# Kernel optimization log

Measured on AMD Instinct MI355X. Metric: run time of the kernel, lower is better.

Reference implementation:

```python
import jax, jax.numpy as jnp
import numpy as np

NP_, NC_, E_, F_, D_, O_ = 50000, 100000, 600000, 69, 128, 2


def _embed(x, shift, scale, w1, b1, w2, b2):
    # PreNormLayer (shift+scale) -> Linear -> ReLU -> Linear -> ReLU
    x = (x + shift) * scale
    return jax.nn.relu(jax.nn.relu(x @ w1 + b1) @ w2 + b2)


def _biconv(left, src, dst, right, wl, bl, wr, sf, wf, bf, sp, wo1, bo1, wo2, bo2):
    # message: final( left_mod(right[dst]) + right_mod(left[src]) ), mean-scatter to dst
    pre = (right[dst] @ wl + bl) + left[src] @ wr            # [E, D]
    msg = jax.nn.relu(pre * sf) @ wf + bf                    # [E, D]
    n = right.shape[0]
    sums = jax.ops.segment_sum(msg, dst, num_segments=n)     # [N_right, D]
    cnt = jax.ops.segment_sum(jnp.ones((dst.shape[0], 1), msg.dtype), dst, num_segments=n)
    agg = sums / jnp.maximum(cnt, 1.0)
    h = jnp.concatenate([agg * sp, right], axis=-1)          # [N_right, 2D]
    return jax.nn.relu(h @ wo1 + bo1) @ wo2 + bo2


def setup_inputs():
    key = jax.random.key(0)
    ks = jax.random.split(key, 40)
    it = iter(range(4, 40))
    def nw(shape):
        return (jax.random.normal(ks[next(it)], shape, dtype=jnp.float32) * 0.05)
    inp = {}
    inp['pivot_features'] = jax.random.normal(ks[0], (NP_, F_), dtype=jnp.float32)
    inp['children_features'] = jax.random.normal(ks[1], (NC_, F_), dtype=jnp.float32)
    src = jax.random.randint(ks[2], (E_,), 0, NP_, dtype=jnp.int32)
    dst = jax.random.randint(ks[3], (E_,), 0, NC_, dtype=jnp.int32)
    inp['edge_indices'] = jnp.stack([src, dst], axis=0)
    # pivot / children embedding MLPs (PreNorm buffers at init values)
    for p in ('pe', 'ce'):
        inp[p + '_shift'] = jnp.zeros((F_,), jnp.float32)
        inp[p + '_scale'] = jnp.ones((F_,), jnp.float32)
        inp[p + '_w1'] = nw((F_, D_)); inp[p + '_b1'] = jnp.zeros((D_,), jnp.float32)
        inp[p + '_w2'] = nw((D_, D_)); inp[p + '_b2'] = jnp.zeros((D_,), jnp.float32)
    # two bipartite conv layers
    for p in ('vc', 'cv'):
        inp[p + '_wl'] = nw((D_, D_)); inp[p + '_bl'] = jnp.zeros((D_,), jnp.float32)
        inp[p + '_wr'] = nw((D_, D_))
        inp[p + '_sf'] = jnp.ones((1,), jnp.float32)   # PreNormLayer(1, shift=False) scale
        inp[p + '_wf'] = nw((D_, D_)); inp[p + '_bf'] = jnp.zeros((D_,), jnp.float32)
        inp[p + '_sp'] = jnp.ones((1,), jnp.float32)   # post_conv PreNormLayer scale
        inp[p + '_wo1'] = nw((2 * D_, D_)); inp[p + '_bo1'] = jnp.zeros((D_,), jnp.float32)
        inp[p + '_wo2'] = nw((D_, D_)); inp[p + '_bo2'] = jnp.zeros((D_,), jnp.float32)
    inp['out_w1'] = nw((D_, D_)); inp['out_b1'] = jnp.zeros((D_,), jnp.float32)
    inp['out_w2'] = nw((D_, O_)); inp['out_b2'] = jnp.zeros((O_,), jnp.float32)
    return inp


def reference(pivot_features, children_features, edge_indices,
              pe_shift, pe_scale, pe_w1, pe_b1, pe_w2, pe_b2,
              ce_shift, ce_scale, ce_w1, ce_b1, ce_w2, ce_b2,
              vc_wl, vc_bl, vc_wr, vc_sf, vc_wf, vc_bf, vc_sp, vc_wo1, vc_bo1, vc_wo2, vc_bo2,
              cv_wl, cv_bl, cv_wr, cv_sf, cv_wf, cv_bf, cv_sp, cv_wo1, cv_bo1, cv_wo2, cv_bo2,
              out_w1, out_b1, out_w2, out_b2):
    pv = _embed(pivot_features, pe_shift, pe_scale, pe_w1, pe_b1, pe_w2, pe_b2)
    ch = _embed(children_features, ce_shift, ce_scale, ce_w1, ce_b1, ce_w2, ce_b2)
    src, dst = edge_indices[0], edge_indices[1]
    # conv_v_to_c: left=pivot, right=children, aggregate to children
    ch = _biconv(pv, src, dst, ch, vc_wl, vc_bl, vc_wr, vc_sf, vc_wf, vc_bf, vc_sp,
                 vc_wo1, vc_bo1, vc_wo2, vc_bo2)
    # conv_c_to_v with reversed edges: left=children, right=pivot, aggregate to pivot
    pv = _biconv(ch, dst, src, pv, cv_wl, cv_bl, cv_wr, cv_sf, cv_wf, cv_bf, cv_sp,
                 cv_wo1, cv_bo1, cv_wo2, cv_bo2)
    return jax.nn.sigmoid(jax.nn.relu(pv @ out_w1 + out_b1) @ out_w2 + out_b2)
```

## Files before the change

kernel.cpp:

```cpp
#include <hip/hip_runtime.h>
#include <math.h>


typedef unsigned short u16;
typedef __attribute__((ext_vector_type(8))) short s8v;
typedef __attribute__((ext_vector_type(4))) float f4v;

__device__ __forceinline__ float bf2f(u16 u) {
    unsigned x = ((unsigned)u) << 16;
    return __builtin_bit_cast(float, x);
}
__device__ __forceinline__ u16 f2bf(float f) {
    unsigned x = __builtin_bit_cast(unsigned, f);
    unsigned r = x + 0x7fffu + ((x >> 16) & 1u);
    return (u16)(r >> 16);
}
__device__ __forceinline__ void unpack8(uint4 u, float* f) {
    f[0] = bf2f((u16)(u.x & 0xffff)); f[1] = bf2f((u16)(u.x >> 16));
    f[2] = bf2f((u16)(u.y & 0xffff)); f[3] = bf2f((u16)(u.y >> 16));
    f[4] = bf2f((u16)(u.z & 0xffff)); f[5] = bf2f((u16)(u.z >> 16));
    f[6] = bf2f((u16)(u.w & 0xffff)); f[7] = bf2f((u16)(u.w >> 16));
}

struct SmEnt { const float* A; const float* B; const float* s; };
struct SmPack { SmEnt e[4]; };

__global__ __launch_bounds__(256) void smallmm(SmPack p, float* __restrict__ out)
{
    int t = blockIdx.x * 256 + threadIdx.x;
    int m = t >> 14;
    int o = t & 16383;
    int i = o >> 7, j = o & 127;
    SmEnt en = p.e[m];
    float acc = 0.f;
#pragma unroll 4
    for (int k = 0; k < 128; ++k) acc += en.A[i * 128 + k] * en.B[k * 128 + j];
    if (en.s) acc *= *en.s;
    out[(size_t)m * 16384 + o] = acc;
}

__global__ void vecpre(
    const float* vc_bf, const float* vc_wo1, const float* vc_sp,
    const float* cv_bf, const float* cv_wo1, const float* cv_sp,
    const float* vc_bo2, const float* cv_wr,
    const float* cv_bo2, const float* out_w1, const float* out_b1,
    float* __restrict__ vout)
{
    int j = threadIdx.x;
    if (j >= 128) return;
    float a0 = 0.f, a1 = 0.f, a2 = 0.f, a3 = 0.f;
    for (int k = 0; k < 128; ++k) {
        a0 += vc_bf[k] * vc_wo1[k * 128 + j];
        a1 += cv_bf[k] * cv_wo1[k * 128 + j];
        a2 += vc_bo2[k] * cv_wr[k * 128 + j];
        a3 += cv_bo2[k] * out_w1[k * 128 + j];
    }
    vout[j] = a0 * (*vc_sp);
    vout[128 + j] = a1 * (*cv_sp);
    vout[256 + j] = a2;
    vout[384 + j] = a3 + out_b1[j];
}

struct WEnt { const float* src; int Ksrc; int Kdst; };
struct WPack { WEnt e[14]; };

__global__ __launch_bounds__(256) void wconvert(WPack p, u16* __restrict__ wt)
{
    int t = blockIdx.x * 256 + threadIdx.x;
    int m = t >> 15;
    int i = t & 32767;
    WEnt en = p.e[m];
    if (i >= (en.Kdst << 7)) return;
    int k = i >> 7, col = i & 127;
    float v = (k < en.Ksrc) ? en.src[k * 128 + col] : 0.f;
    wt[(size_t)m * 32768 + (size_t)col * en.Kdst + k] = f2bf(v);
}

__global__ __launch_bounds__(256) void featconv(
    const float* __restrict__ x, const float* __restrict__ shift,
    const float* __restrict__ scale, u16* __restrict__ y,
    long total, int F)
{
    for (long i = (long)blockIdx.x * 256 + threadIdx.x; i < total;
         i += (long)gridDim.x * 256) {
        int c = (int)(i % 96);
        long r = i / 96;
        float v = 0.f;
        if (c < F) {
            v = x[r * F + c];
            v = (v + shift[c]) * scale[c];
        }
        y[i] = f2bf(v);
    }
}

template <int KS1, bool HASA2, bool RELU, bool GATE>
__global__ __launch_bounds__(256) void gemm_rb(
    const u16* __restrict__ A1, const u16* __restrict__ A2,
    const u16* __restrict__ WT1,
    const u16* __restrict__ WT2,
    const float* __restrict__ bias0,
    const float* __restrict__ bias1,
    const float* __restrict__ gate,
    u16* __restrict__ out, int M)
{
    constexpr int K1 = KS1 * 32;
    constexpr bool PF = !HASA2;
    constexpr int AS = KS1 + (HASA2 ? 4 : 0);
    const int lane = threadIdx.x & 63;
    const int c = lane & 15;
    const int kg = lane >> 4;
    const int wid = blockIdx.x * 4 + (threadIdx.x >> 6);
    const int ws = gridDim.x * 4;
    const int items = M >> 4;

    const u16* wbase = WT1 + (size_t)c * K1 + kg * 8;
    s8v bp[KS1][8];
#pragma unroll
    for (int ks = 0; ks < KS1; ++ks)
#pragma unroll
        for (int nt = 0; nt < 8; ++nt)
            bp[ks][nt] = *(const s8v*)(wbase + ((size_t)nt * 16) * K1 + ks * 32);

    const u16* wbase2 = HASA2 ? (WT2 + (size_t)c * 128 + kg * 8) : nullptr;

    float bc0[8], bc1[8];
#pragma unroll
    for (int nt = 0; nt < 8; ++nt) {
        bc0[nt] = bias0 ? bias0[nt * 16 + c] : 0.f;
        bc1[nt] = (GATE && bias1) ? bias1[nt * 16 + c] : 0.f;
    }

    auto lda = [&](s8v* a, int item) {
        const u16* ap = A1 + (size_t)((item << 4) + c) * K1 + kg * 8;
#pragma unroll
        for (int ks = 0; ks < KS1; ++ks) a[ks] = *(const s8v*)(ap + ks * 32);
        if (HASA2) {
            const u16* ap2 = A2 + (size_t)((item << 4) + c) * 128 + kg * 8;
#pragma unroll
            for (int ks = 0; ks < 4; ++ks) a[KS1 + ks] = *(const s8v*)(ap2 + ks * 32);
        }
    };

    s8v a[AS], an[AS], a2[AS];
    int item = wid;
    if (item < items) lda(a, item);
    if (PF && item + ws < items) lda(an, item + ws);
    while (item < items) {
        const int i2 = item + 2 * ws;
        if (PF && i2 < items) lda(a2, i2);

        f4v acc[8];
#pragma unroll
        for (int nt = 0; nt < 8; ++nt) acc[nt] = (f4v){0.f, 0.f, 0.f, 0.f};
#pragma unroll
        for (int ks = 0; ks < KS1; ++ks)
#pragma unroll
            for (int nt = 0; nt < 8; ++nt)
                acc[nt] = __builtin_amdgcn_mfma_f32_16x16x32_bf16(a[ks], bp[ks][nt], acc[nt], 0, 0, 0);
        if (HASA2) {
#pragma unroll
            for (int ks = 0; ks < 4; ++ks)
#pragma unroll
                for (int nt = 0; nt < 8; ++nt) {
                    s8v b = *(const s8v*)(wbase2 + ((size_t)nt * 16) * 128 + ks * 32);
                    acc[nt] = __builtin_amdgcn_mfma_f32_16x16x32_bf16(a[KS1 + ks], b, acc[nt], 0, 0, 0);
                }
        }

        const int r0 = item << 4;
        float g4[4];
#pragma unroll
        for (int j = 0; j < 4; ++j)
            g4[j] = GATE ? (gate[r0 + kg * 4 + j] > 0.f ? 1.f : 0.f) : 0.f;
#pragma unroll
        for (int nt = 0; nt < 8; ++nt)
#pragma unroll
            for (int j = 0; j < 4; ++j) {
                float v = acc[nt][j] + bc0[nt] + g4[j] * bc1[nt];
                if (RELU) v = fmaxf(v, 0.f);
                out[(size_t)(r0 + kg * 4 + j) * 128 + nt * 16 + c] = f2bf(v);
            }

        if (PF) {
#pragma unroll
            for (int ks = 0; ks < AS; ++ks) { a[ks] = an[ks]; an[ks] = a2[ks]; }
        } else if (item + ws < items) {
            lda(a, item + ws);
        }
        item += ws;
    }
}

__global__ __launch_bounds__(256) void head_fused(
    const u16* __restrict__ A1, const u16* __restrict__ WT,
    const float* __restrict__ b1, const float* __restrict__ w2,
    const float* __restrict__ b2, float* __restrict__ outp, int M)
{
    constexpr int KT = 128;
    const int lane = threadIdx.x & 63;
    const int c = lane & 15;
    const int kg = lane >> 4;
    const int wid = blockIdx.x * 4 + (threadIdx.x >> 6);
    const int ws = gridDim.x * 4;
    const int items = M >> 4;

    const u16* wbase = WT + (size_t)c * KT + kg * 8;
    s8v bp[4][8];
#pragma unroll
    for (int ks = 0; ks < 4; ++ks)
#pragma unroll
        for (int nt = 0; nt < 8; ++nt)
            bp[ks][nt] = *(const s8v*)(wbase + ((size_t)nt * 16) * KT + ks * 32);

    float bc[8], w2c0[8], w2c1[8];
#pragma unroll
    for (int nt = 0; nt < 8; ++nt) {
        int col = nt * 16 + c;
        bc[nt] = b1[col];
        w2c0[nt] = w2[col * 2 + 0];
        w2c1[nt] = w2[col * 2 + 1];
    }
    const float s0 = b2[0], s1 = b2[1];

    for (int item = wid; item < items; item += ws) {
        const int r0 = item << 4;
        const u16* ap = A1 + (size_t)(r0 + c) * 128 + kg * 8;
        s8v a[4];
#pragma unroll
        for (int ks = 0; ks < 4; ++ks) a[ks] = *(const s8v*)(ap + ks * 32);

        f4v acc[8];
#pragma unroll
        for (int nt = 0; nt < 8; ++nt) acc[nt] = (f4v){0.f, 0.f, 0.f, 0.f};
#pragma unroll
        for (int ks = 0; ks < 4; ++ks)
#pragma unroll
            for (int nt = 0; nt < 8; ++nt)
                acc[nt] = __builtin_amdgcn_mfma_f32_16x16x32_bf16(a[ks], bp[ks][nt], acc[nt], 0, 0, 0);

        float pp0[4] = {0.f, 0.f, 0.f, 0.f}, pp1[4] = {0.f, 0.f, 0.f, 0.f};
#pragma unroll
        for (int nt = 0; nt < 8; ++nt)
#pragma unroll
            for (int j = 0; j < 4; ++j) {
                float v = fmaxf(acc[nt][j] + bc[nt], 0.f);
                pp0[j] += v * w2c0[nt];
                pp1[j] += v * w2c1[nt];
            }
#pragma unroll
        for (int m = 1; m < 16; m <<= 1)
#pragma unroll
            for (int j = 0; j < 4; ++j) {
                pp0[j] += __shfl_xor(pp0[j], m);
                pp1[j] += __shfl_xor(pp1[j], m);
            }
        if (c == 0) {
#pragma unroll
            for (int j = 0; j < 4; ++j) {
                int row = r0 + kg * 4 + j;
                outp[(size_t)row * 2 + 0] = 1.f / (1.f + expf(-(pp0[j] + s0)));
                outp[(size_t)row * 2 + 1] = 1.f / (1.f + expf(-(pp1[j] + s1)));
            }
        }
    }
}


__global__ __launch_bounds__(256) void binA(
    const int* __restrict__ src, const int* __restrict__ dst,
    int E, int CH, int NB, int nbk_c, int NBK,
    int* __restrict__ G, int* __restrict__ Tb)
{
    __shared__ int h[1024];
    const int blk = blockIdx.x, tid = threadIdx.x;
    for (int i = tid; i < NBK; i += 256) h[i] = 0;
    __syncthreads();
    const int e0 = blk * CH, e1 = min(E, e0 + CH);
    for (int e = e0 + tid; e < e1; e += 256) {
        atomicAdd(&h[dst[e] >> 9], 1);
        atomicAdd(&h[nbk_c + (src[e] >> 9)], 1);
    }
    __syncthreads();
    for (int b = tid; b < NBK; b += 256) {
        const int v = h[b];
        G[b * NB + blk] = v;
        if (v) atomicAdd(&Tb[b], v);
    }
}

__global__ __launch_bounds__(512) void binS(
    const int* __restrict__ Tb, int NBK, int* __restrict__ BB)
{
    __shared__ int wsum[8];
    const int tid = threadIdx.x;
    const int T = (tid < NBK) ? Tb[tid] : 0;
    const int lane = tid & 63, wv = tid >> 6;
    int incl = T;
#pragma unroll
    for (int d = 1; d < 64; d <<= 1) {
        int up = __shfl_up(incl, d);
        if (lane >= d) incl += up;
    }
    if (lane == 63) wsum[wv] = incl;
    __syncthreads();
    if (tid == 0) {
        int run = 0;
        for (int w = 0; w < 8; ++w) { int t = wsum[w]; wsum[w] = run; run += t; }
    }
    __syncthreads();
    const int base = wsum[wv] + incl - T;
    if (tid < NBK) {
        BB[tid] = base;
        if (tid == NBK - 1) BB[NBK] = base + T;
    }
}

__global__ __launch_bounds__(64) void binP(
    const int* __restrict__ G, const int* __restrict__ BB,
    int NB, int* __restrict__ PBB)
{
    const int b = blockIdx.x, l = threadIdx.x;
    const int* g = G + (size_t)b * NB;
    const int v0 = (l < NB) ? g[l] : 0;
    const int v1 = (l + 64 < NB) ? g[l + 64] : 0;
    int i0 = v0, i1 = v1;
#pragma unroll
    for (int d = 1; d < 64; d <<= 1) {
        int u0 = __shfl_up(i0, d);
        int u1 = __shfl_up(i1, d);
        if (l >= d) { i0 += u0; i1 += u1; }
    }
    const int t0 = __shfl(i0, 63);
    const int base = BB[b];
    int* p = PBB + (size_t)b * NB;
    if (l < NB) p[l] = base + i0 - v0;
    if (l + 64 < NB) p[l + 64] = base + t0 + i1 - v1;
}

__global__ __launch_bounds__(256) void binB(
    const int* __restrict__ src, const int* __restrict__ dst,
    int E, int CH, int NB, int nbk_c, int NBK,
    const int* __restrict__ PBB, unsigned* __restrict__ REC)
{
    __shared__ int fill[1024];
    const int blk = blockIdx.x, tid = threadIdx.x;
    for (int i = tid; i < NBK; i += 256) fill[i] = 0;
    __syncthreads();
    const int e0 = blk * CH, e1 = min(E, e0 + CH);
    for (int e = e0 + tid; e < e1; e += 256) {
        const int s = src[e], d = dst[e];
        const int bc = d >> 9;
        const int pc = PBB[bc * NB + blk] + atomicAdd(&fill[bc], 1);
        REC[pc] = (unsigned)s | ((unsigned)(d & 511) << 17);
        const int bp = nbk_c + (s >> 9);
        const int pp = PBB[bp * NB + blk] + atomicAdd(&fill[bp], 1);
        REC[pp] = (unsigned)d | ((unsigned)(s & 511) << 17);
    }
}

__global__ __launch_bounds__(256) void binC(
    const unsigned* __restrict__ REC, const int* __restrict__ BB,
    int bucket_base, int Nn,
    int* __restrict__ off_out, int* __restrict__ cnt_out, int* __restrict__ AJ)
{
    __shared__ int nh[512], lo[512], fl[512], ws2[4];
    const int b = blockIdx.x, tid = threadIdx.x;
    const int gb = bucket_base + b;
    const int r0 = BB[gb], r1 = BB[gb + 1];
    const int node0 = b << 9;
    const int kmax = min(512, Nn - node0);
    nh[tid] = 0; nh[tid + 256] = 0;
    fl[tid] = 0; fl[tid + 256] = 0;
    __syncthreads();
    for (int i = r0 + tid; i < r1; i += 256)
        atomicAdd(&nh[REC[i] >> 17], 1);
    __syncthreads();
    const int v0 = nh[2 * tid], v1 = nh[2 * tid + 1];
    const int s = v0 + v1;
    const int lane = tid & 63, wv = tid >> 6;
    int incl = s;
#pragma unroll
    for (int d = 1; d < 64; d <<= 1) {
        int up = __shfl_up(incl, d);
        if (lane >= d) incl += up;
    }
    if (lane == 63) ws2[wv] = incl;
    __syncthreads();
    if (tid == 0) {
        int run = 0;
        for (int w = 0; w < 4; ++w) { int t = ws2[w]; ws2[w] = run; run += t; }
    }
    __syncthreads();
    const int base = ws2[wv] + incl - s;
    lo[2 * tid] = base;
    lo[2 * tid + 1] = base + v0;
    __syncthreads();
    for (int k = tid; k < kmax; k += 256) {
        off_out[node0 + k] = r0 + lo[k];
        cnt_out[node0 + k] = nh[k];
    }
    for (int i = r0 + tid; i < r1; i += 256) {
        const unsigned rec = REC[i];
        const int k = rec >> 17;
        const int pos = r0 + lo[k] + atomicAdd(&fl[k], 1);
        AJ[pos] = (int)(rec & 0x1FFFFu);
    }
}

__global__ __launch_bounds__(256) void node_gather2(
    const int* __restrict__ off, const int* __restrict__ cnt,
    const int* __restrict__ adj,
    const u16* __restrict__ RW, const u16* __restrict__ LW,
    u16* __restrict__ Sdiv, float* __restrict__ cntf,
    const float* __restrict__ sf_p, int N)
{
    int t = blockIdx.x * 256 + threadIdx.x;
    int n = t >> 5;
    if (n >= N) return;
    int l32 = t & 31;
    int c = l32 & 15;
    int half = l32 >> 4;
    const float sf = *sf_p;
    const int start = off[n], len = cnt[n];

    float rw[8];
    unpack8(*(const uint4*)(RW + (size_t)n * 128 + c * 8), rw);
    float acc[8] = {0.f, 0.f, 0.f, 0.f, 0.f, 0.f, 0.f, 0.f};

    for (int i = half; i < len; i += 2) {
        int l = adj[start + i];
        float lw[8];
        unpack8(*(const uint4*)(LW + (size_t)l * 128 + c * 8), lw);
#pragma unroll
        for (int j = 0; j < 8; ++j)
            acc[j] += fmaxf((rw[j] + lw[j]) * sf, 0.f);
    }
#pragma unroll
    for (int j = 0; j < 8; ++j) acc[j] += __shfl_xor(acc[j], 16);

    if (half == 0) {
        float inv = 1.f / fmaxf((float)len, 1.f);
        uint4 o;
        o.x = (unsigned)f2bf(acc[0] * inv) | ((unsigned)f2bf(acc[1] * inv) << 16);
        o.y = (unsigned)f2bf(acc[2] * inv) | ((unsigned)f2bf(acc[3] * inv) << 16);
        o.z = (unsigned)f2bf(acc[4] * inv) | ((unsigned)f2bf(acc[5] * inv) << 16);
        o.w = (unsigned)f2bf(acc[6] * inv) | ((unsigned)f2bf(acc[7] * inv) << 16);
        *(uint4*)(Sdiv + (size_t)n * 128 + c * 8) = o;
        if (l32 == 0) cntf[n] = (float)len;
    }
}

extern "C" void kernel_launch(void* const* d_in, const int* in_sizes, int n_in,
                              void* d_out, int out_size, void* d_ws, size_t ws_size,
                              hipStream_t stream)
{
    const float* pivot = (const float*)d_in[0];
    const float* child = (const float*)d_in[1];
    const int* edges = (const int*)d_in[2];
    const int F = in_sizes[3];
    const int NP = in_sizes[0] / F;
    const int NC = in_sizes[1] / F;
    const int E = in_sizes[2] / 2;
    const int* src = edges;
    const int* dst = edges + E;

    const float *pe_shift = (const float*)d_in[3], *pe_scale = (const float*)d_in[4],
                *pe_w1 = (const float*)d_in[5], *pe_b1 = (const float*)d_in[6],
                *pe_w2 = (const float*)d_in[7], *pe_b2 = (const float*)d_in[8];
    const float *ce_shift = (const float*)d_in[9], *ce_scale = (const float*)d_in[10],
                *ce_w1 = (const float*)d_in[11], *ce_b1 = (const float*)d_in[12],
                *ce_w2 = (const float*)d_in[13], *ce_b2 = (const float*)d_in[14];
    const float *vc_wl = (const float*)d_in[15], *vc_bl = (const float*)d_in[16],
                *vc_wr = (const float*)d_in[17], *vc_sf = (const float*)d_in[18],
                *vc_wf = (const float*)d_in[19], *vc_bf = (const float*)d_in[20],
                *vc_sp = (const float*)d_in[21], *vc_wo1 = (const float*)d_in[22],
                *vc_bo1 = (const float*)d_in[23], *vc_wo2 = (const float*)d_in[24],
                *vc_bo2 = (const float*)d_in[25];
    const float *cv_wl = (const float*)d_in[26], *cv_bl = (const float*)d_in[27],
                *cv_wr = (const float*)d_in[28], *cv_sf = (const float*)d_in[29],
                *cv_wf = (const float*)d_in[30], *cv_bf = (const float*)d_in[31],
                *cv_sp = (const float*)d_in[32], *cv_wo1 = (const float*)d_in[33],
                *cv_bo1 = (const float*)d_in[34], *cv_wo2 = (const float*)d_in[35],
                *cv_bo2 = (const float*)d_in[36];
    const float *out_w1 = (const float*)d_in[37], *out_b1 = (const float*)d_in[38],
                *out_w2 = (const float*)d_in[39], *out_b2 = (const float*)d_in[40];

    char* base = (char*)d_ws;
    size_t off = 0;
    auto carve = [&](size_t bytes) {
        void* p = base + off;
        off += (bytes + 255) & ~(size_t)255;
        return p;
    };
    float* Wsc = (float*)carve((size_t)4 * 16384 * 4);
    float* Vsc = (float*)carve((size_t)4 * 128 * 4);
    u16* WT = (u16*)carve((size_t)14 * 32768 * 2);
    u16* FP = (u16*)carve((size_t)NP * 96 * 2);
    u16* FC = (u16*)carve((size_t)NC * 96 * 2);
    u16* B0 = (u16*)carve((size_t)NP * 128 * 2);
    u16* B1 = (u16*)carve((size_t)NC * 128 * 2);
    u16* B2 = (u16*)carve((size_t)NC * 128 * 2);
    u16* B3 = (u16*)carve((size_t)NC * 128 * 2);
    u16* B4 = (u16*)carve((size_t)NC * 128 * 2);
    const int NMAX = (NC > NP) ? NC : NP;
    float* cntf = (float*)carve((size_t)NMAX * 4);

    const int NB = 120;
    const int CH = (E + NB - 1) / NB;
    const int nbk_c = (NC + 511) >> 9;
    const int nbk_p = (NP + 511) >> 9;
    const int NBK = nbk_c + nbk_p;
    int* cnt_c = (int*)carve((size_t)NC * 4);
    int* cnt_p = (int*)carve((size_t)NP * 4);
    int* off_c = (int*)carve((size_t)NC * 4);
    int* off_p = (int*)carve((size_t)NP * 4);
    int* G = (int*)carve((size_t)NBK * NB * 4);
    int* PBB = (int*)carve((size_t)NBK * NB * 4);
    int* BB = (int*)carve((size_t)(NBK + 1) * 4);
    int* Tb = (int*)carve((size_t)NBK * 4);
    unsigned* REC = (unsigned*)carve((size_t)2 * E * 4);
    int* AJ = (int*)carve((size_t)2 * E * 4);

    SmPack sp;
    sp.e[0] = {vc_wf, vc_wo1, vc_sp};
    sp.e[1] = {cv_wf, cv_wo1, cv_sp};
    sp.e[2] = {vc_wo2, cv_wr, nullptr};
    sp.e[3] = {cv_wo2, out_w1, nullptr};
    hipLaunchKernelGGL(smallmm, dim3(256), dim3(256), 0, stream, sp, Wsc);
    hipLaunchKernelGGL(vecpre, dim3(1), dim3(128), 0, stream,
                       vc_bf, vc_wo1, vc_sp, cv_bf, cv_wo1, cv_sp,
                       vc_bo2, cv_wr, cv_bo2, out_w1, out_b1, Vsc);
    const float* cvec_vc = Vsc;
    const float* cvec_cv = Vsc + 128;
    const float* cx = Vsc + 256;
    const float* bh = Vsc + 384;

    WPack wp;
    auto setw = [&](int i, const float* s, int ks, int kd) {
        wp.e[i].src = s; wp.e[i].Ksrc = ks; wp.e[i].Kdst = kd;
    };
    setw(0, pe_w1, F, 96);            setw(1, pe_w2, 128, 128);
    setw(2, ce_w1, F, 96);            setw(3, ce_w2, 128, 128);
    setw(4, vc_wl, 128, 128);         setw(5, vc_wr, 128, 128);
    setw(6, Wsc + 0 * 16384, 128, 128);
    setw(7, vc_wo1 + 128 * 128, 128, 128);
    setw(8, Wsc + 2 * 16384, 128, 128);
    setw(9, cv_wl, 128, 128);         setw(10, cv_wr, 128, 128);
    setw(11, Wsc + 1 * 16384, 128, 128);
    setw(12, cv_wo1 + 128 * 128, 128, 128);
    setw(13, Wsc + 3 * 16384, 128, 128);
    hipLaunchKernelGGL(wconvert, dim3(14 * 128), dim3(256), 0, stream, wp, WT);
    auto wt = [&](int i) { return WT + (size_t)i * 32768; };

    hipLaunchKernelGGL(featconv, dim3(2048), dim3(256), 0, stream,
                       pivot, pe_shift, pe_scale, FP, (long)NP * 96, F);
    hipLaunchKernelGGL(featconv, dim3(2048), dim3(256), 0, stream,
                       child, ce_shift, ce_scale, FC, (long)NC * 96, F);

    hipMemsetAsync(Tb, 0, (size_t)NBK * 4, stream);
    hipLaunchKernelGGL(binA, dim3(NB), dim3(256), 0, stream,
                       src, dst, E, CH, NB, nbk_c, NBK, G, Tb);
    hipLaunchKernelGGL(binS, dim3(1), dim3(512), 0, stream, Tb, NBK, BB);
    hipLaunchKernelGGL(binP, dim3(NBK), dim3(64), 0, stream, G, BB, NB, PBB);
    hipLaunchKernelGGL(binB, dim3(NB), dim3(256), 0, stream,
                       src, dst, E, CH, NB, nbk_c, NBK, PBB, REC);
    hipLaunchKernelGGL(binC, dim3(nbk_c), dim3(256), 0, stream,
                       REC, BB, 0, NC, off_c, cnt_c, AJ);
    hipLaunchKernelGGL(binC, dim3(nbk_p), dim3(256), 0, stream,
                       REC, BB, nbk_c, NP, off_p, cnt_p, AJ);

    const dim3 blk(256);
    auto grd = [](int M) {
        int items = M >> 4;
        int b = (items + 3) / 4;
        return dim3((unsigned)(b < 512 ? b : 512));
    };

    gemm_rb<3, false, true, false><<<grd(NP), blk, 0, stream>>>(
        FP, nullptr, wt(0), nullptr, pe_b1, nullptr, nullptr, B1, NP);
    gemm_rb<4, false, true, false><<<grd(NP), blk, 0, stream>>>(
        B1, nullptr, wt(1), nullptr, pe_b2, nullptr, nullptr, B0, NP);
    gemm_rb<3, false, true, false><<<grd(NC), blk, 0, stream>>>(
        FC, nullptr, wt(2), nullptr, ce_b1, nullptr, nullptr, B1, NC);
    gemm_rb<4, false, true, false><<<grd(NC), blk, 0, stream>>>(
        B1, nullptr, wt(3), nullptr, ce_b2, nullptr, nullptr, B2, NC);

    gemm_rb<4, false, false, false><<<grd(NC), blk, 0, stream>>>(
        B2, nullptr, wt(4), nullptr, vc_bl, nullptr, nullptr, B1, NC);
    gemm_rb<4, false, false, false><<<grd(NP), blk, 0, stream>>>(
        B0, nullptr, wt(5), nullptr, nullptr, nullptr, nullptr, B3, NP);
    hipLaunchKernelGGL(node_gather2, dim3(((size_t)NC * 32 + 255) / 256), blk, 0,
                       stream, off_c, cnt_c, AJ, B1, B3, B4, cntf, vc_sf, NC);
    gemm_rb<4, true, true, true><<<grd(NC), blk, 0, stream>>>(
        B4, B2, wt(6), wt(7), vc_bo1, cvec_vc, cntf, B1, NC);
    gemm_rb<4, false, false, false><<<grd(NC), blk, 0, stream>>>(
        B1, nullptr, wt(8), nullptr, cx, nullptr, nullptr, B3, NC);

    gemm_rb<4, false, false, false><<<grd(NP), blk, 0, stream>>>(
        B0, nullptr, wt(9), nullptr, cv_bl, nullptr, nullptr, B2, NP);
    hipLaunchKernelGGL(node_gather2, dim3(((size_t)NP * 32 + 255) / 256), blk, 0,
                       stream, off_p, cnt_p, AJ, B2, B3, B4, cntf, cv_sf, NP);
    gemm_rb<4, true, true, true><<<grd(NP), blk, 0, stream>>>(
        B4, B0, wt(11), wt(12), cv_bo1, cvec_cv, cntf, B1, NP);

    hipLaunchKernelGGL(head_fused, grd(NP), blk, 0, stream,
                       B1, wt(13), bh, out_w2, out_b2, (float*)d_out, NP);
}
```

Before: 362.0 us.

## Batch independent GEMMs into multi-job launches and transpose MFMA for packed stores

Independent per-node GEMMs (pivot and children embeddings, and the three projection GEMMs) are grouped into single launches using blockIdx.y as a job selector. The two feature-conversion kernels and the two binC kernels are merged the same way, which cuts launch count and improves GPU fill for the smaller pivot jobs. The MFMA operands are swapped so each lane holds four consecutive output columns, allowing packed 8-byte bf16 stores and vector bias loads instead of scattered 2-byte stores. Extra buffers are allocated to avoid aliasing between the now-concurrent jobs.

After: 373.7 us. +3.2%, slower.

```diff
diff --git a/kernel.cpp b/kernel.cpp
--- a/kernel.cpp
+++ b/kernel.cpp
@@ -14,6 +14,9 @@
     unsigned x = __builtin_bit_cast(unsigned, f);
     unsigned r = x + 0x7fffu + ((x >> 16) & 1u);
     return (u16)(r >> 16);
+}
+__device__ __forceinline__ unsigned pk2(float a, float b) {
+    return (unsigned)f2bf(a) | ((unsigned)f2bf(b) << 16);
 }
 __device__ __forceinline__ void unpack8(uint4 u, float* f) {
     f[0] = bf2f((u16)(u.x & 0xffff)); f[1] = bf2f((u16)(u.x >> 16));
@@ -76,19 +79,24 @@
     wt[(size_t)m * 32768 + (size_t)col * en.Kdst + k] = f2bf(v);
 }
 
-__global__ __launch_bounds__(256) void featconv(
-    const float* __restrict__ x, const float* __restrict__ shift,
-    const float* __restrict__ scale, u16* __restrict__ y,
-    long total, int F)
+__global__ __launch_bounds__(256) void featconv2(
+    const float* __restrict__ pv, const float* __restrict__ ch,
+    const float* __restrict__ psh, const float* __restrict__ psc,
+    const float* __restrict__ csh, const float* __restrict__ csc,
+    u16* __restrict__ y, long NPr, long total, int F)
 {
     for (long i = (long)blockIdx.x * 256 + threadIdx.x; i < total;
          i += (long)gridDim.x * 256) {
-        int c = (int)(i % 96);
+        int cc = (int)(i % 96);
         long r = i / 96;
+        const float *x, *sh, *sc;
+        long row;
+        if (r < NPr) { x = pv; sh = psh; sc = psc; row = r; }
+        else { x = ch; sh = csh; sc = csc; row = r - NPr; }
         float v = 0.f;
-        if (c < F) {
-            v = x[r * F + c];
-            v = (v + shift[c]) * scale[c];
+        if (cc < F) {
+            v = x[row * F + cc];
+            v = (v + sh[cc]) * sc[cc];
         }
         y[i] = f2bf(v);
     }
@@ -124,12 +132,11 @@
 
     const u16* wbase2 = HASA2 ? (WT2 + (size_t)c * 128 + kg * 8) : nullptr;
 
-    float bc0[8], bc1[8];
-#pragma unroll
-    for (int nt = 0; nt < 8; ++nt) {
-        bc0[nt] = bias0 ? bias0[nt * 16 + c] : 0.f;
-        bc1[nt] = (GATE && bias1) ? bias1[nt * 16 + c] : 0.f;
-    }
+    f4v bq[8];
+#pragma unroll
+    for (int nt = 0; nt < 8; ++nt)
+        bq[nt] = bias0 ? *(const f4v*)(bias0 + nt * 16 + kg * 4)
+                       : (f4v){0.f, 0.f, 0.f, 0.f};
 
     auto lda = [&](s8v* a, int item) {
         const u16* ap = A1 + (size_t)((item << 4) + c) * K1 + kg * 8;
@@ -157,30 +164,40 @@
         for (int ks = 0; ks < KS1; ++ks)
 #pragma unroll
             for (int nt = 0; nt < 8; ++nt)
-                acc[nt] = __builtin_amdgcn_mfma_f32_16x16x32_bf16(a[ks], bp[ks][nt], acc[nt], 0, 0, 0);
+                acc[nt] = __builtin_amdgcn_mfma_f32_16x16x32_bf16(bp[ks][nt], a[ks], acc[nt], 0, 0, 0);
         if (HASA2) {
 #pragma unroll
             for (int ks = 0; ks < 4; ++ks)
 #pragma unroll
                 for (int nt = 0; nt < 8; ++nt) {
                     s8v b = *(const s8v*)(wbase2 + ((size_t)nt * 16) * 128 + ks * 32);
-                    acc[nt] = __builtin_amdgcn_mfma_f32_16x16x32_bf16(a[KS1 + ks], b, acc[nt], 0, 0, 0);
+                    acc[nt] = __builtin_amdgcn_mfma_f32_16x16x32_bf16(b, a[KS1 + ks], acc[nt], 0, 0, 0);
                 }
         }
 
         const int r0 = item << 4;
-        float g4[4];
-#pragma unroll
-        for (int j = 0; j < 4; ++j)
-            g4[j] = GATE ? (gate[r0 + kg * 4 + j] > 0.f ? 1.f : 0.f) : 0.f;
-#pragma unroll
-        for (int nt = 0; nt < 8; ++nt)
-#pragma unroll
-            for (int j = 0; j < 4; ++j) {
-                float v = acc[nt][j] + bc0[nt] + g4[j] * bc1[nt];
-                if (RELU) v = fmaxf(v, 0.f);
-                out[(size_t)(r0 + kg * 4 + j) * 128 + nt * 16 + c] = f2bf(v);
+        const float g = GATE ? (gate[r0 + c] > 0.f ? 1.f : 0.f) : 0.f;
+        u16* op = out + (size_t)(r0 + c) * 128 + kg * 4;
+#pragma unroll
+        for (int nt = 0; nt < 8; ++nt) {
+            float v0 = acc[nt][0] + bq[nt][0];
+            float v1 = acc[nt][1] + bq[nt][1];
+            float v2 = acc[nt][2] + bq[nt][2];
+            float v3 = acc[nt][3] + bq[nt][3];
+            if (GATE && bias1) {
+                f4v b1q = *(const f4v*)(bias1 + nt * 16 + kg * 4);
+                v0 += g * b1q[0]; v1 += g * b1q[1];
+                v2 += g * b1q[2]; v3 += g * b1q[3];
             }
+            if (RELU) {
+                v0 = fmaxf(v0, 0.f); v1 = fmaxf(v1, 0.f);
+                v2 = fmaxf(v2, 0.f); v3 = fmaxf(v3, 0.f);
+            }
+            uint2 pkv;
+            pkv.x = pk2(v0, v1);
+            pkv.y = pk2(v2, v3);
+            *(uint2*)(op + nt * 16) = pkv;
+        }
 
         if (PF) {
 #pragma unroll
@@ -188,6 +205,85 @@
         } else if (item + ws < items) {
             lda(a, item + ws);
         }
+        item += ws;
+    }
+}
+
+struct GJob { const u16* A1; const u16* WT1; const float* bias0; u16* out; int M; };
+struct GJobs3 { GJob j[3]; };
+
+template <int KS1, bool RELU>
+__global__ __launch_bounds__(256) void gemm_multi(GJobs3 jobs)
+{
+    constexpr int K1 = KS1 * 32;
+    const GJob jb = jobs.j[blockIdx.y];
+    const u16* __restrict__ A1 = jb.A1;
+    const float* __restrict__ bias0 = jb.bias0;
+    u16* __restrict__ out = jb.out;
+    const int lane = threadIdx.x & 63;
+    const int c = lane & 15;
+    const int kg = lane >> 4;
+    const int wid = blockIdx.x * 4 + (threadIdx.x >> 6);
+    const int ws = gridDim.x * 4;
+    const int items = jb.M >> 4;
+
+    const u16* wbase = jb.WT1 + (size_t)c * K1 + kg * 8;
+    s8v bp[KS1][8];
+#pragma unroll
+    for (int ks = 0; ks < KS1; ++ks)
+#pragma unroll
+        for (int nt = 0; nt < 8; ++nt)
+            bp[ks][nt] = *(const s8v*)(wbase + ((size_t)nt * 16) * K1 + ks * 32);
+
+    f4v bq[8];
+#pragma unroll
+    for (int nt = 0; nt < 8; ++nt)
+        bq[nt] = bias0 ? *(const f4v*)(bias0 + nt * 16 + kg * 4)
+                       : (f4v){0.f, 0.f, 0.f, 0.f};
+
+    auto lda = [&](s8v* a, int item) {
+        const u16* ap = A1 + (size_t)((item << 4) + c) * K1 + kg * 8;
+#pragma unroll
+        for (int ks = 0; ks < KS1; ++ks) a[ks] = *(const s8v*)(ap + ks * 32);
+    };
+
+    s8v a[KS1], an[KS1], a2[KS1];
+    int item = wid;
+    if (item < items) lda(a, item);
+    if (item + ws < items) lda(an, item + ws);
+    while (item < items) {
+        const int i2 = item + 2 * ws;
+        if (i2 < items) lda(a2, i2);
+
+        f4v acc[8];
+#pragma unroll
+        for (int nt = 0; nt < 8; ++nt) acc[nt] = (f4v){0.f, 0.f, 0.f, 0.f};
+#pragma unroll
+        for (int ks = 0; ks < KS1; ++ks)
+#pragma unroll
+            for (int nt = 0; nt < 8; ++nt)
+                acc[nt] = __builtin_amdgcn_mfma_f32_16x16x32_bf16(bp[ks][nt], a[ks], acc[nt], 0, 0, 0);
+
+        const int r0 = item << 4;
+        u16* op = out + (size_t)(r0 + c) * 128 + kg * 4;
+#pragma unroll
+        for (int nt = 0; nt < 8; ++nt) {
+            float v0 = acc[nt][0] + bq[nt][0];
+            float v1 = acc[nt][1] + bq[nt][1];
+            float v2 = acc[nt][2] + bq[nt][2];
+            float v3 = acc[nt][3] + bq[nt][3];
+            if (RELU) {
+                v0 = fmaxf(v0, 0.f); v1 = fmaxf(v1, 0.f);
+                v2 = fmaxf(v2, 0.f); v3 = fmaxf(v3, 0.f);
+            }
+            uint2 pkv;
+            pkv.x = pk2(v0, v1);
+            pkv.y = pk2(v2, v3);
+            *(uint2*)(op + nt * 16) = pkv;
+        }
+
+#pragma unroll
+        for (int ks = 0; ks < KS1; ++ks) { a[ks] = an[ks]; an[ks] = a2[ks]; }
         item += ws;
     }
 }
@@ -213,14 +309,10 @@
         for (int nt = 0; nt < 8; ++nt)
             bp[ks][nt] = *(const s8v*)(wbase + ((size_t)nt * 16) * KT + ks * 32);
 
-    float bc[8], w2c0[8], w2c1[8];
-#pragma unroll
-    for (int nt = 0; nt < 8; ++nt) {
-        int col = nt * 16 + c;
-        bc[nt] = b1[col];
-        w2c0[nt] = w2[col * 2 + 0];
-        w2c1[nt] = w2[col * 2 + 1];
-    }
+    f4v bhq[8];
+#pragma unroll
+    for (int nt = 0; nt < 8; ++nt)
+        bhq[nt] = *(const f4v*)(b1 + nt * 16 + kg * 4);
     const float s0 = b2[0], s1 = b2[1];
 
     for (int item = wid; item < items; item += ws) {
@@ -237,35 +329,30 @@
         for (int ks = 0; ks < 4; ++ks)
 #pragma unroll
             for (int nt = 0; nt < 8; ++nt)
-                acc[nt] = __builtin_amdgcn_mfma_f32_16x16x32_bf16(a[ks], bp[ks][nt], acc[nt], 0, 0, 0);
-
-        float pp0[4] = {0.f, 0.f, 0.f, 0.f}, pp1[4] = {0.f, 0.f, 0.f, 0.f};
-#pragma unroll
-        for (int nt = 0; nt < 8; ++nt)
-#pragma unroll
-            for (int j = 0; j < 4; ++j) {
-                float v = fmaxf(acc[nt][j] + bc[nt], 0.f);
-                pp0[j] += v * w2c0[nt];
-                pp1[j] += v * w2c1[nt];
-            }
-#pragma unroll
-        for (int m = 1; m < 16; m <<= 1)
-#pragma unroll
-            for (int j = 0; j < 4; ++j) {
-                pp0[j] += __shfl_xor(pp0[j], m);
-                pp1[j] += __shfl_xor(pp1[j], m);
-            }
-        if (c == 0) {
-#pragma unroll
-            for (int j = 0; j < 4; ++j) {
-                int row = r0 + kg * 4 + j;
-                outp[(size_t)row * 2 + 0] = 1.f / (1.f + expf(-(pp0[j] + s0)));
-                outp[(size_t)row * 2 + 1] = 1.f / (1.f + expf(-(pp1[j] + s1)));
-            }
+                acc[nt] = __builtin_amdgcn_mfma_f32_16x16x32_bf16(bp[ks][nt], a[ks], acc[nt], 0, 0, 0);
+
+        float p0 = 0.f, p1 = 0.f;
+#pragma unroll
+        for (int nt = 0; nt < 8; ++nt) {
+            float v0 = fmaxf(acc[nt][0] + bhq[nt][0], 0.f);
+            float v1 = fmaxf(acc[nt][1] + bhq[nt][1], 0.f);
+            float v2 = fmaxf(acc[nt][2] + bhq[nt][2], 0.f);
+            float v3 = fmaxf(acc[nt][3] + bhq[nt][3], 0.f);
+            const float4 wa = *(const float4*)(w2 + (nt * 16 + kg * 4) * 2);
+            const float4 wb = *(const float4*)(w2 + (nt * 16 + kg * 4) * 2 + 4);
+            p0 += v0 * wa.x + v1 * wa.z + v2 * wb.x + v3 * wb.z;
+            p1 += v0 * wa.y + v1 * wa.w + v2 * wb.y + v3 * wb.w;
         }
-    }
-}
-
+        p0 += __shfl_xor(p0, 16); p0 += __shfl_xor(p0, 32);
+        p1 += __shfl_xor(p1, 16); p1 += __shfl_xor(p1, 32);
+        if (kg == 0) {
+            float2 o;
+            o.x = 1.f / (1.f + expf(-(p0 + s0)));
+            o.y = 1.f / (1.f + expf(-(p1 + s1)));
+            *(float2*)(outp + (size_t)(r0 + c) * 2) = o;
+        }
+    }
+}
 
 __global__ __launch_bounds__(256) void binA(
     const int* __restrict__ src, const int* __restrict__ dst,
@@ -359,16 +446,19 @@
     }
 }
 
-__global__ __launch_bounds__(256) void binC(
+__global__ __launch_bounds__(256) void binC2(
     const unsigned* __restrict__ REC, const int* __restrict__ BB,
-    int bucket_base, int Nn,
-    int* __restrict__ off_out, int* __restrict__ cnt_out, int* __restrict__ AJ)
+    int nbk_c, int NCn, int NPn,
+    int* __restrict__ off_c, int* __restrict__ cnt_c,
+    int* __restrict__ off_p, int* __restrict__ cnt_p, int* __restrict__ AJ)
 {
     __shared__ int nh[512], lo[512], fl[512], ws2[4];
     const int b = blockIdx.x, tid = threadIdx.x;
-    const int gb = bucket_base + b;
-    const int r0 = BB[gb], r1 = BB[gb + 1];
-    const int node0 = b << 9;
+    int Nn, node0;
+    int *off_out, *cnt_out;
+    if (b < nbk_c) { Nn = NCn; node0 = b << 9; off_out = off_c; cnt_out = cnt_c; }
+    else { Nn = NPn; node0 = (b - nbk_c) << 9; off_out = off_p; cnt_out = cnt_p; }
+    const int r0 = BB[b], r1 = BB[b + 1];
     const int kmax = min(512, Nn - node0);
     nh[tid] = 0; nh[tid + 256] = 0;
     fl[tid] = 0; fl[tid + 256] = 0;
@@ -442,10 +532,10 @@
     if (half == 0) {
         float inv = 1.f / fmaxf((float)len, 1.f);
         uint4 o;
-        o.x = (unsigned)f2bf(acc[0] * inv) | ((unsigned)f2bf(acc[1] * inv) << 16);
-        o.y = (unsigned)f2bf(acc[2] * inv) | ((unsigned)f2bf(acc[3] * inv) << 16);
-        o.z = (unsigned)f2bf(acc[4] * inv) | ((unsigned)f2bf(acc[5] * inv) << 16);
-        o.w = (unsigned)f2bf(acc[6] * inv) | ((unsigned)f2bf(acc[7] * inv) << 16);
+        o.x = pk2(acc[0] * inv, acc[1] * inv);
+        o.y = pk2(acc[2] * inv, acc[3] * inv);
+        o.z = pk2(acc[4] * inv, acc[5] * inv);
+        o.w = pk2(acc[6] * inv, acc[7] * inv);
         *(uint4*)(Sdiv + (size_t)n * 128 + c * 8) = o;
         if (l32 == 0) cntf[n] = (float)len;
     }
@@ -496,13 +586,16 @@
     float* Wsc = (float*)carve((size_t)4 * 16384 * 4);
     float* Vsc = (float*)carve((size_t)4 * 128 * 4);
     u16* WT = (u16*)carve((size_t)14 * 32768 * 2);
-    u16* FP = (u16*)carve((size_t)NP * 96 * 2);
-    u16* FC = (u16*)carve((size_t)NC * 96 * 2);
+    u16* FPC = (u16*)carve((size_t)(NP + NC) * 96 * 2);
+    u16* FP = FPC;
+    u16* FC = FPC + (size_t)NP * 96;
     u16* B0 = (u16*)carve((size_t)NP * 128 * 2);
     u16* B1 = (u16*)carve((size_t)NC * 128 * 2);
     u16* B2 = (u16*)carve((size_t)NC * 128 * 2);
     u16* B3 = (u16*)carve((size_t)NC * 128 * 2);
     u16* B4 = (u16*)carve((size_t)NC * 128 * 2);
+    u16* B5 = (u16*)carve((size_t)NC * 128 * 2);
+    u16* B6 = (u16*)carve((size_t)NP * 128 * 2);
     const int NMAX = (NC > NP) ? NC : NP;
     float* cntf = (float*)carve((size_t)NMAX * 4);
 
@@ -553,10 +646,9 @@
     hipLaunchKernelGGL(wconvert, dim3(14 * 128), dim3(256), 0, stream, wp, WT);
     auto wt = [&](int i) { return WT + (size_t)i * 32768; };
 
-    hipLaunchKernelGGL(featconv, dim3(2048), dim3(256), 0, stream,
-                       pivot, pe_shift, pe_scale, FP, (long)NP * 96, F);
-    hipLaunchKernelGGL(featconv, dim3(2048), dim3(256), 0, stream,
-                       child, ce_shift, ce_scale, FC, (long)NC * 96, F);
+    hipLaunchKernelGGL(featconv2, dim3(2048), dim3(256), 0, stream,
+                       pivot, child, pe_shift, pe_scale, ce_shift, ce_scale,
+                       FPC, (long)NP, (long)(NP + NC) * 96, F);
 
     hipMemsetAsync(Tb, 0, (size_t)NBK * 4, stream);
     hipLaunchKernelGGL(binA, dim3(NB), dim3(256), 0, stream,
@@ -565,10 +657,8 @@
     hipLaunchKernelGGL(binP, dim3(NBK), dim3(64), 0, stream, G, BB, NB, PBB);
     hipLaunchKernelGGL(binB, dim3(NB), dim3(256), 0, stream,
                        src, dst, E, CH, NB, nbk_c, NBK, PBB, REC);
-    hipLaunchKernelGGL(binC, dim3(nbk_c), dim3(256), 0, stream,
-                       REC, BB, 0, NC, off_c, cnt_c, AJ);
-    hipLaunchKernelGGL(binC, dim3(nbk_p), dim3(256), 0, stream,
-                       REC, BB, nbk_c, NP, off_p, cnt_p, AJ);
+    hipLaunchKernelGGL(binC2, dim3(NBK), dim3(256), 0, stream,
+                       REC, BB, nbk_c, NC, NP, off_c, cnt_c, off_p, cnt_p, AJ);
 
     const dim3 blk(256);
     auto grd = [](int M) {
@@ -577,30 +667,40 @@
         return dim3((unsigned)(b < 512 ? b : 512));
     };
 
-    gemm_rb<3, false, true, false><<<grd(NP), blk, 0, stream>>>(
-        FP, nullptr, wt(0), nullptr, pe_b1, nullptr, nullptr, B1, NP);
-    gemm_rb<4, false, true, false><<<grd(NP), blk, 0, stream>>>(
-        B1, nullptr, wt(1), nullptr, pe_b2, nullptr, nullptr, B0, NP);
-    gemm_rb<3, false, true, false><<<grd(NC), blk, 0, stream>>>(
-        FC, nullptr, wt(2), nullptr, ce_b1, nullptr, nullptr, B1, NC);
-    gemm_rb<4, false, true, false><<<grd(NC), blk, 0, stream>>>(
-        B1, nullptr, wt(3), nullptr, ce_b2, nullptr, nullptr, B2, NC);
-
-    gemm_rb<4, false, false, false><<<grd(NC), blk, 0, stream>>>(
-        B2, nullptr, wt(4), nullptr, vc_bl, nullptr, nullptr, B1, NC);
-    gemm_rb<4, false, false, false><<<grd(NP), blk, 0, stream>>>(
-        B0, nullptr, wt(5), nullptr, nullptr, nullptr, nullptr, B3, NP);
+    {
+        GJobs3 j;
+        j.j[0] = {FP, wt(0), pe_b1, B1, NP};
+        j.j[1] = {FC, wt(2), ce_b1, B5, NC};
+        j.j[2] = j.j[0];
+        dim3 g = grd(NC); g.y = 2;
+        hipLaunchKernelGGL(HIP_KERNEL_NAME(gemm_multi<3, true>), g, blk, 0, stream, j);
+    }
+    {
+        GJobs3 j;
+        j.j[0] = {B1, wt(1), pe_b2, B0, NP};
+        j.j[1] = {B5, wt(3), ce_b2, B2, NC};
+        j.j[2] = j.j[0];
+        dim3 g = grd(NC); g.y = 2;
+        hipLaunchKernelGGL(HIP_KERNEL_NAME(gemm_multi<4, true>), g, blk, 0, stream, j);
+    }
+    {
+        GJobs3 j;
+        j.j[0] = {B2, wt(4), vc_bl, B1, NC};
+        j.j[1] = {B0, wt(5), nullptr, B3, NP};
+        j.j[2] = {B0, wt(9), cv_bl, B6, NP};
+        dim3 g = grd(NC); g.y = 3;
+        hipLaunchKernelGGL(HIP_KERNEL_NAME(gemm_multi<4, false>), g, blk, 0, stream, j);
+    }
+
     hipLaunchKernelGGL(node_gather2, dim3(((size_t)NC * 32 + 255) / 256), blk, 0,
                        stream, off_c, cnt_c, AJ, B1, B3, B4, cntf, vc_sf, NC);
     gemm_rb<4, true, true, true><<<grd(NC), blk, 0, stream>>>(
-        B4, B2, wt(6), wt(7), vc_bo1, cvec_vc, cntf, B1, NC);
+        B4, B2, wt(6), wt(7), vc_bo1, cvec_vc, cntf, B5, NC);
     gemm_rb<4, false, false, false><<<grd(NC), blk, 0, stream>>>(
-        B1, nullptr, wt(8), nullptr, cx, nullptr, nullptr, B3, NC);
-
-    gemm_rb<4, false, false, false><<<grd(NP), blk, 0, stream>>>(
-        B0, nullptr, wt(9), nullptr, cv_bl, nullptr, nullptr, B2, NP);
+        B5, nullptr, wt(8), nullptr, cx, nullptr, nullptr, B3, NC);
+
     hipLaunchKernelGGL(node_gather2, dim3(((size_t)NP * 32 + 255) / 256), blk, 0,
-                       stream, off_p, cnt_p, AJ, B2, B3, B4, cntf, cv_sf, NP);
+                       stream, off_p, cnt_p, AJ, B6, B3, B4, cntf, cv_sf, NP);
     gemm_rb<4, true, true, true><<<grd(NP), blk, 0, stream>>>(
         B4, B0, wt(11), wt(12), cv_bo1, cvec_cv, cntf, B1, NP);
 
```
